# Kernel tuning notes

Hardware: AMD Instinct MI355X
Metric: run time of the kernel (lower is better)

Reference implementation:

```python
import jax, jax.numpy as jnp
import numpy as np

D_MODEL = 512
NHEAD = 8
MAX_REL = 256  # max_relative_position


def _linear(x, w, b):
    # torch nn.Linear: y = x @ W^T + b, W: [out, in]
    return jnp.einsum('...i,oi->...o', x, w) + b


def setup_inputs() -> dict:
    key = jax.random.key(0)
    ks = jax.random.split(key, 16)
    B, S, D = 32, 512, D_MODEL
    s = 0.02
    inp = {
        'query': jax.random.normal(ks[0], (B, S, D), jnp.float32),
        'key':   jax.random.normal(ks[1], (B, S, D), jnp.float32),
        'value': jax.random.normal(ks[2], (B, S, D), jnp.float32),
        # local attention projections (torch Linear weights [out,in])
        'wq': jax.random.normal(ks[3], (D, D), jnp.float32) * s,
        'bq': jnp.zeros((D,), jnp.float32),
        'wk': jax.random.normal(ks[4], (D, D), jnp.float32) * s,
        'bk': jnp.zeros((D,), jnp.float32),
        'wv': jax.random.normal(ks[5], (D, D), jnp.float32) * s,
        'bv': jnp.zeros((D,), jnp.float32),
        'wo': jax.random.normal(ks[6], (D, D), jnp.float32) * s,
        'bo': jnp.zeros((D,), jnp.float32),
        # relative-position key embedding table [2*MAX_REL+1, head_dim]
        'rel_k': jax.random.normal(ks[7], (2 * MAX_REL + 1, D // NHEAD), jnp.float32) * s,
        # global nn.MultiheadAttention (nhead//2 heads): packed in_proj + out_proj
        'g_in_w': jax.random.normal(ks[8], (3 * D, D), jnp.float32) * s,
        'g_in_b': jnp.zeros((3 * D,), jnp.float32),
        'g_out_w': jax.random.normal(ks[9], (D, D), jnp.float32) * s,
        'g_out_b': jnp.zeros((D,), jnp.float32),
    }
    return inp


def reference(query, key, value, wq, bq, wk, bk, wv, bv, wo, bo, rel_k,
              g_in_w, g_in_b, g_out_w, g_out_b):
    B, S, D = query.shape
    H, hd = NHEAD, D // NHEAD

    # --- local attention with relative-position bias ---
    q = _linear(query, wq, bq).reshape(B, S, H, hd).transpose(0, 2, 1, 3)  # [B,H,S,hd]
    k = _linear(key,   wk, bk).reshape(B, S, H, hd).transpose(0, 2, 1, 3)
    v = _linear(value, wv, bv).reshape(B, S, H, hd).transpose(0, 2, 1, 3)

    scores = jnp.einsum('bhqd,bhkd->bhqk', q, k) / jnp.sqrt(jnp.float32(hd))

    # relative positions: distance[i,j] = j - i, clamped, shifted to [0, 2*MAX_REL]
    idx = jnp.arange(S)
    rel_ids = jnp.clip(idx[None, :] - idx[:, None], -MAX_REL, MAX_REL) + MAX_REL  # [S,S]
    rel_pos_k = rel_k[rel_ids]  # [S, S, hd]
    scores = scores + jnp.einsum('bhld,lrd->bhlr', q, rel_pos_k)

    attn = jax.nn.softmax(scores, axis=-1)
    local = jnp.einsum('bhqk,bhkd->bhqd', attn, v)
    local = local.transpose(0, 2, 1, 3).reshape(B, S, D)

    # --- global MHA with H//2 heads ---
    Hg = H // 2
    hdg = D // Hg
    qg = _linear(query, g_in_w[:D], g_in_b[:D]).reshape(B, S, Hg, hdg).transpose(0, 2, 1, 3)
    kg = _linear(key,   g_in_w[D:2 * D], g_in_b[D:2 * D]).reshape(B, S, Hg, hdg).transpose(0, 2, 1, 3)
    vg = _linear(value, g_in_w[2 * D:], g_in_b[2 * D:]).reshape(B, S, Hg, hdg).transpose(0, 2, 1, 3)
    gs = jnp.einsum('bhqd,bhkd->bhqk', qg, kg) / jnp.sqrt(jnp.float32(hdg))
    ga = jax.nn.softmax(gs, axis=-1)
    g = jnp.einsum('bhqk,bhkd->bhqd', ga, vg).transpose(0, 2, 1, 3).reshape(B, S, D)
    g = _linear(g, g_out_w, g_out_b)

    combined = 0.7 * local + 0.3 * g
    return _linear(combined, wo, bo)
```

## Files before the change

### kernel.cpp

```cpp
#include <hip/hip_runtime.h>

typedef __attribute__((ext_vector_type(8))) short bh8;
typedef __attribute__((ext_vector_type(4))) float f4;

#define DEVI static __device__ __forceinline__

DEVI unsigned short f2b(float f) {
  union { float f; unsigned u; } v; v.f = f;
  unsigned r = v.u + 0x7fffu + ((v.u >> 16) & 1u);
  return (unsigned short)(r >> 16);
}
DEVI float b2f(unsigned short h) {
  union { unsigned u; float f; } v; v.u = ((unsigned)h) << 16;
  return v.f;
}
DEVI f4 mfma16(bh8 a, bh8 b, f4 c) {
  return __builtin_amdgcn_mfma_f32_16x16x32_bf16(a, b, c, 0, 0, 0);
}
DEVI void gload_lds16(const unsigned short* g, unsigned short* l) {
  __builtin_amdgcn_global_load_lds(
      (const __attribute__((address_space(1))) void*)(g),
      (__attribute__((address_space(3))) void*)(l), 16, 0, 0);
}

__global__ __launch_bounds__(256) void prep_all_kern(
    const float* __restrict__ q, const float* __restrict__ k, const float* __restrict__ v,
    const float* __restrict__ wq, const float* __restrict__ wk, const float* __restrict__ wv,
    const float* __restrict__ g_in_w, const float* __restrict__ g_out_w,
    const float* __restrict__ wo, const float* __restrict__ rel_k,
    const float* __restrict__ bgo, const float* __restrict__ bo,
    unsigned short* __restrict__ xq, unsigned short* __restrict__ xk, unsigned short* __restrict__ xv,
    unsigned short* __restrict__ Wq, unsigned short* __restrict__ Wk, unsigned short* __restrict__ Wv,
    unsigned short* __restrict__ Wo_, unsigned short* __restrict__ WgoT,
    unsigned short* __restrict__ Bfin, unsigned short* __restrict__ Rk,
    float* __restrict__ bias2) {
  if (blockIdx.x < 8192) {
    long i = ((long)blockIdx.x * 256 + threadIdx.x) * 4;
    float4 a = *(const float4*)(q + i);
    float4 b = *(const float4*)(k + i);
    float4 c = *(const float4*)(v + i);
    union { unsigned short s[4]; uint2 u; } pa, pb, pc;
    pa.s[0] = f2b(a.x); pa.s[1] = f2b(a.y); pa.s[2] = f2b(a.z); pa.s[3] = f2b(a.w);
    pb.s[0] = f2b(b.x); pb.s[1] = f2b(b.y); pb.s[2] = f2b(b.z); pb.s[3] = f2b(b.w);
    pc.s[0] = f2b(c.x); pc.s[1] = f2b(c.y); pc.s[2] = f2b(c.z); pc.s[3] = f2b(c.w);
    *(uint2*)(xq + i) = pa.u;
    *(uint2*)(xk + i) = pb.u;
    *(uint2*)(xv + i) = pc.u;
    return;
  }
  int bw = blockIdx.x - 8192;
  if (bw >= 2337) {
    int o = (bw - 2337) * 256 + threadIdx.x;
    if (o < 512) {
      const float* r = wo + (long)o * 512;
      float s = 0.f;
#pragma unroll 4
      for (int m = 0; m < 512; m += 4) {
        float4 a = *(const float4*)(r + m);
        float4 b = *(const float4*)(bgo + m);
        s += a.x * b.x + a.y * b.y + a.z * b.z + a.w * b.w;
      }
      bias2[o] = bo[o] + 0.3f * s;
    }
    return;
  }
  long i = ((long)bw * 256 + threadIdx.x) * 4;
  if (i >= 2392128L) return;
  if (i >= 2097152L && i < 2359296L) {
    long off = i - 2097152L;
    int ii = (int)(off >> 9), p = (int)(off & 511);
    union { unsigned short s[4]; uint2 u; } w;
#pragma unroll
    for (int tt = 0; tt < 4; tt++) w.s[tt] = f2b(g_out_w[(p + tt) * 512 + ii]);
    *(uint2*)(WgoT + off) = w.u;
    return;
  }
  const float* src; unsigned short* dst; long off; float sc = 1.0f;
  if (i < 524288L)        { dst = Wq;  off = i; src = (i < 262144L) ? wq + i : g_in_w + (i - 262144L); }
  else if (i < 1048576L)  { long j = i - 524288L;  dst = Wk;  off = j; src = (j < 262144L) ? wk + j : g_in_w + j; }
  else if (i < 1572864L)  { long j = i - 1048576L; dst = Wv;  off = j; src = (j < 262144L) ? wv + j : g_in_w + 262144L + j; }
  else if (i < 1835008L)  { long j = i - 1572864L; dst = Wo_; off = j; src = wo + j; }
  else if (i < 2097152L)  { long j = i - 1835008L; int col = (int)(j >> 9), kk = (int)(j & 511);
                            dst = Bfin; off = (long)col * 1024 + kk; src = wo + j; sc = 0.7f; }
  else                    { long j = i - 2359296L; dst = Rk;  off = j; src = rel_k + j; }
  float4 f = *(const float4*)src;
  union { unsigned short s[4]; uint2 u; } p;
  p.s[0] = f2b(f.x * sc); p.s[1] = f2b(f.y * sc); p.s[2] = f2b(f.z * sc); p.s[3] = f2b(f.w * sc);
  *(uint2*)(dst + off) = p.u;
}

__global__ __launch_bounds__(256) void gemm3_kern(
    const unsigned short* __restrict__ Xq, const unsigned short* __restrict__ Xk,
    const unsigned short* __restrict__ Xv,
    const unsigned short* __restrict__ Wq, const unsigned short* __restrict__ Wk,
    const unsigned short* __restrict__ Wv,
    const float* __restrict__ bq, const float* __restrict__ bk, const float* __restrict__ bv,
    const float* __restrict__ g_in_b,
    unsigned short* __restrict__ Yq, unsigned short* __restrict__ Yk_,
    unsigned short* __restrict__ Yvt_l, unsigned short* __restrict__ Yvt_g,
    const unsigned short* __restrict__ Wo_, const unsigned short* __restrict__ WgoT,
    unsigned short* __restrict__ Bfin) {
  __shared__ unsigned short lsA[128 * 64];
  __shared__ unsigned short lsB[128 * 64];
  const int t = threadIdx.x;
  const int lane = t & 63, w = t >> 6;
  const int l15 = lane & 15, g = lane >> 4, g4 = g * 4;
  const int n = blockIdx.x;

  const unsigned short *Ap, *Bp;
  const float *b0 = nullptr, *b1 = nullptr;
  int seg, rb, cb;
  if (n < 3072) {
    seg = n >> 10;
    int m = n & 1023;
    int x = m >> 3, c = m & 7;
    rb = (c * 16 + (x & 15)) * 128;
    cb = (x >> 4) * 128;
    Ap = (seg == 0) ? Xq : (seg == 1) ? Xk : Xv;
    Bp = (seg == 0) ? Wq : (seg == 1) ? Wk : Wv;
    b0 = (seg == 0) ? bq : (seg == 1) ? bk : bv;
    b1 = g_in_b + seg * 512;
  } else {
    seg = 3;
    int m2 = n - 3072;
    rb = (m2 & 3) * 128; cb = (m2 >> 2) * 128;
    Ap = Wo_; Bp = WgoT;
  }

  const int wr = (w >> 1) * 64, wc = (w & 1) * 64;
  const int tr = t >> 3;
  const int kci = ((t & 7) ^ (tr & 7)) * 8;
  const unsigned short* pa = Ap + (long)(rb + tr) * 512 + kci;
  const unsigned short* pb = Bp + (long)(cb + tr) * 512 + kci;

  f4 acc[4][4] = {};
  for (int k0 = 0; k0 < 512; k0 += 64) {
    __syncthreads();
#pragma unroll
    for (int p = 0; p < 4; p++) {
      gload_lds16(pa + k0 + (long)p * 32 * 512, lsA + p * 2048 + w * 512);
      gload_lds16(pb + k0 + (long)p * 32 * 512, lsB + p * 2048 + w * 512);
    }
    __syncthreads();
    bh8 af[2][4], bf[2][4];
#pragma unroll
    for (int kh = 0; kh < 2; kh++) {
#pragma unroll
      for (int m = 0; m < 4; m++) {
        int rl = wr + m * 16 + l15;
        af[kh][m] = *(const bh8*)(lsA + rl * 64 + (((kh * 4 + g) ^ (rl & 7)) * 8));
      }
#pragma unroll
      for (int nn = 0; nn < 4; nn++) {
        int rl = wc + nn * 16 + l15;
        bf[kh][nn] = *(const bh8*)(lsB + rl * 64 + (((kh * 4 + g) ^ (rl & 7)) * 8));
      }
    }
    __builtin_amdgcn_s_setprio(1);
#pragma unroll
    for (int m = 0; m < 4; m++)
#pragma unroll
      for (int nn = 0; nn < 4; nn++) {
        acc[m][nn] = mfma16(af[0][m], bf[0][nn], acc[m][nn]);
        acc[m][nn] = mfma16(af[1][m], bf[1][nn], acc[m][nn]);
      }
    __builtin_amdgcn_s_setprio(0);
  }

  if (seg == 3) {
#pragma unroll
    for (int m = 0; m < 4; m++)
#pragma unroll
      for (int nn = 0; nn < 4; nn++)
#pragma unroll
        for (int j = 0; j < 4; j++) {
          int row = rb + wr + m * 16 + g4 + j;
          int col = cb + wc + nn * 16 + l15;
          Bfin[(long)row * 1024 + 512 + col] = f2b(0.3f * acc[m][nn][j]);
        }
    return;
  }
  if (seg == 2) {
#pragma unroll
    for (int m = 0; m < 4; m++)
#pragma unroll
      for (int nn = 0; nn < 4; nn++) {
        int col = cb + wc + nn * 16 + l15;
        float bsv = (col < 512) ? b0[col] : b1[col - 512];
        unsigned r[4];
#pragma unroll
        for (int j = 0; j < 4; j++) {
          union { float f; unsigned u; } v; v.f = acc[m][nn][j] + bsv;
          r[j] = v.u + 0x7fffu + ((v.u >> 16) & 1u);
        }
        unsigned lo = (r[0] >> 16) | (r[1] & 0xffff0000u);
        unsigned hi = (r[2] >> 16) | (r[3] & 0xffff0000u);
        int row0 = rb + wr + m * 16 + g4;
        int bb = row0 >> 9, s = row0 & 511;
        if (col < 512) {
          int hh = col >> 6, d = col & 63;
          *(uint2*)(Yvt_l + (((long)(bb * 8 + hh) * 64 + d) << 9) + s) = make_uint2(lo, hi);
        } else {
          int c2 = col - 512, hg = c2 >> 7, dg = c2 & 127;
          *(uint2*)(Yvt_g + (((long)(bb * 4 + hg) * 128 + dg) << 9) + s) = make_uint2(lo, hi);
        }
      }
    return;
  }
  unsigned short* Yo = (seg == 0) ? Yq : Yk_;
#pragma unroll
  for (int m = 0; m < 4; m++)
#pragma unroll
    for (int nn = 0; nn < 4; nn++)
#pragma unroll
      for (int j = 0; j < 4; j++) {
        int row = rb + wr + m * 16 + g4 + j;
        int col = cb + wc + nn * 16 + l15;
        float v = acc[m][nn][j] + ((col < 512) ? b0[col] : b1[col - 512]);
        Yo[(long)row * 1024 + col] = f2b(v);
      }
}

__global__ __launch_bounds__(256) void gemm_fin_kern(
    const unsigned short* __restrict__ A, const unsigned short* __restrict__ Bw,
    const float* __restrict__ bias0, float* __restrict__ outf) {
  __shared__ unsigned short lsA[128 * 64];
  __shared__ unsigned short lsB[128 * 64];
  const int t = threadIdx.x;
  const int lane = t & 63, w = t >> 6;
  const int l15 = lane & 15, g = lane >> 4, g4 = g * 4;
  int n = blockIdx.x;
  int x = n >> 3, c = n & 7;
  const int rb = (c * 16 + (x & 15)) * 128;
  const int cb = (x >> 4) * 128;
  const int wr = (w >> 1) * 64, wc = (w & 1) * 64;
  const int tr = t >> 3;
  const int kci = ((t & 7) ^ (tr & 7)) * 8;

  const unsigned short* pa = A + (long)(rb + tr) * 1024 + kci;
  const unsigned short* pb = Bw + (long)(cb + tr) * 1024 + kci;

  f4 acc[4][4] = {};
  for (int k0 = 0; k0 < 1024; k0 += 64) {
    __syncthreads();
#pragma unroll
    for (int p = 0; p < 4; p++) {
      gload_lds16(pa + k0 + (long)p * 32 * 1024, lsA + p * 2048 + w * 512);
      gload_lds16(pb + k0 + (long)p * 32 * 1024, lsB + p * 2048 + w * 512);
    }
    __syncthreads();
    bh8 af[2][4], bf[2][4];
#pragma unroll
    for (int kh = 0; kh < 2; kh++) {
#pragma unroll
      for (int m = 0; m < 4; m++) {
        int rl = wr + m * 16 + l15;
        af[kh][m] = *(const bh8*)(lsA + rl * 64 + (((kh * 4 + g) ^ (rl & 7)) * 8));
      }
#pragma unroll
      for (int nn = 0; nn < 4; nn++) {
        int rl = wc + nn * 16 + l15;
        bf[kh][nn] = *(const bh8*)(lsB + rl * 64 + (((kh * 4 + g) ^ (rl & 7)) * 8));
      }
    }
    __builtin_amdgcn_s_setprio(1);
#pragma unroll
    for (int m = 0; m < 4; m++)
#pragma unroll
      for (int nn = 0; nn < 4; nn++) {
        acc[m][nn] = mfma16(af[0][m], bf[0][nn], acc[m][nn]);
        acc[m][nn] = mfma16(af[1][m], bf[1][nn], acc[m][nn]);
      }
    __builtin_amdgcn_s_setprio(0);
  }
#pragma unroll
  for (int m = 0; m < 4; m++)
#pragma unroll
    for (int nn = 0; nn < 4; nn++)
#pragma unroll
      for (int j = 0; j < 4; j++) {
        int row = rb + wr + m * 16 + g4 + j;
        int col = cb + wc + nn * 16 + l15;
        outf[(long)row * 512 + col] = acc[m][nn][j] + bias0[col];
      }
}

__global__ __launch_bounds__(512, 4) void attn_local_kern(
    const unsigned short* __restrict__ Yq, const unsigned short* __restrict__ Yk,
    const unsigned short* __restrict__ Yvt, const unsigned short* __restrict__ relk,
    unsigned short* __restrict__ outC) {
  __shared__ unsigned short kv[2][8192];
  __shared__ unsigned short buf[32 * 524];
  __shared__ float redbuf[8][32];

  const int t = threadIdx.x, lane = t & 63, w = t >> 6;
  const int l15 = lane & 15, g = lane >> 4, g8 = g * 8;
  int n = blockIdx.x;
  int bid = (n & 7) * 512 + (n >> 3);
  const int qt = bid & 15;
  const int h = (bid >> 4) & 7;
  const int b = bid >> 7;
  const int qb = qt * 32;
  const long base = ((long)(b * 512)) * 1024 + h * 64;
  const long vbase = ((long)(b * 8 + h)) * 64 * 512;

#define STAGE_K(ROFF, BUF) { \
    const int c_ = t & 7; \
    _Pragma("unroll") \
    for (int it = 0; it < 2; it++) { \
      int rr = it * 64 + (t >> 3); \
      gload_lds16(Yk + base + (long)((ROFF) + rr) * 1024 + ((c_ ^ (rr & 7)) * 8), \
                  kv[BUF] + it * 4096 + w * 512); \
    } }
#define STAGE_V(COFF, BUF) { \
    const int c_ = t & 15; \
    _Pragma("unroll") \
    for (int it = 0; it < 2; it++) { \
      int dd_ = it * 32 + (t >> 4); \
      gload_lds16(Yvt + vbase + (long)dd_ * 512 + (COFF) + ((c_ ^ (dd_ & 15)) * 8), \
                  kv[BUF] + it * 4096 + w * 512); \
    } }
#define QK(CH) { \
    int rl = w * 16 + l15; \
    const unsigned short* kb_ = kv[(CH) & 1]; \
    bh8 k0 = *(const bh8*)(kb_ + rl * 64 + ((g ^ (rl & 7)) * 8)); \
    bh8 k1 = *(const bh8*)(kb_ + rl * 64 + (((g + 4) ^ (rl & 7)) * 8)); \
    _Pragma("unroll") \
    for (int mm = 0; mm < 2; mm++) { \
      f4 a = {}; \
      a = mfma16(qf[mm][0], k0, a); \
      a = mfma16(qf[mm][1], k1, a); \
      sc[mm][CH] = a; \
    } }
#define GATHER(CH) { \
    _Pragma("unroll") \
    for (int mm = 0; mm < 2; mm++) \
    _Pragma("unroll") \
    for (int j = 0; j < 4; j++) { \
      int lr = mm * 16 + g * 4 + j; \
      int rowb = lr * 524; \
      int idx = rowb + 256 - (qb + lr) + (CH) * 128 + w * 16 + l15; \
      idx = idx < rowb ? rowb : idx; \
      idx = idx > rowb + 512 ? rowb + 512 : idx; \
      float p = exp2f(fmaf(sc[mm][CH][j], 0.18033688011112042f, b2f(buf[idx]))); \
      sc[mm][CH][j] = p; \
      rs[mm][j] += p; \
    } }

  STAGE_K(0, 0);

  bh8 qf[2][2];
#pragma unroll
  for (int mm = 0; mm < 2; mm++) {
    const unsigned short* qp = Yq + base + (long)(qb + mm * 16 + l15) * 1024 + g8;
    qf[mm][0] = *(const bh8*)(qp);
    qf[mm][1] = *(const bh8*)(qp + 32);
  }

  for (int tt = w; tt < 33; tt += 8) {
    int ri = tt * 16 + l15; if (ri > 512) ri = 512;
    const unsigned short* rp = relk + ri * 64 + g8;
    bh8 rf0 = *(const bh8*)(rp), rf1 = *(const bh8*)(rp + 32);
    int col = tt * 16 + l15;
#pragma unroll
    for (int mm = 0; mm < 2; mm++) {
      f4 a = {};
      a = mfma16(qf[mm][0], rf0, a);
      a = mfma16(qf[mm][1], rf1, a);
      if (col < 524) {
#pragma unroll
        for (int j = 0; j < 4; j++)
          buf[(mm * 16 + g * 4 + j) * 524 + col] = f2b(a[j] * 1.4426950408889634f);
      }
    }
  }
  __syncthreads();

  f4 sc[2][4];
  float rs[2][4] = {};

#pragma unroll
  for (int c = 0; c < 4; c++) {
    if (c < 3) { STAGE_K((c + 1) * 128, (c + 1) & 1); }
    else       { STAGE_V(0, 0); }
    __builtin_amdgcn_s_setprio(1);
    QK(c);
    __builtin_amdgcn_s_setprio(0);
    GATHER(c);
    __syncthreads();
  }

#pragma unroll
  for (int mm = 0; mm < 2; mm++)
#pragma unroll
    for (int j = 0; j < 4; j++) {
      int lr = mm * 16 + g * 4 + j;
      float s = rs[mm][j];
      for (int d = 1; d < 16; d <<= 1) s += __shfl_xor(s, d, 64);
      if (l15 == 0) redbuf[w][lr] = s;
    }
#pragma unroll
  for (int mm = 0; mm < 2; mm++)
#pragma unroll
    for (int ch = 0; ch < 4; ch++) {
      int col = ch * 128 + w * 16 + l15;
#pragma unroll
      for (int j = 0; j < 4; j++)
        buf[(mm * 16 + g * 4 + j) * 524 + col] = f2b(sc[mm][ch][j]);
    }
  __syncthreads();

  const int mmw = w >> 2, dt = w & 3;
  const int dd = dt * 16 + l15;
  float rinvj[4];
#pragma unroll
  for (int j = 0; j < 4; j++) {
    int lr = mmw * 16 + g * 4 + j;
    float s = 0.f;
#pragma unroll
    for (int ww = 0; ww < 8; ww++) s += redbuf[ww][lr];
    rinvj[j] = __builtin_amdgcn_rcpf(s);
  }

  f4 accO = {};
#pragma unroll
  for (int d = 0; d < 4; d++) {
    if (d < 3) { STAGE_V((d + 1) * 128, (d + 1) & 1); }
    const unsigned short* vb_ = kv[d & 1];
    __builtin_amdgcn_s_setprio(1);
#pragma unroll
    for (int ks2 = 0; ks2 < 4; ks2++) {
      union { uint2 u[2]; bh8 v; } pa;
      const unsigned short* pp = buf + (mmw * 16 + l15) * 524 + (d * 4 + ks2) * 32 + g8;
      pa.u[0] = *(const uint2*)(pp);
      pa.u[1] = *(const uint2*)(pp + 4);
      bh8 vv = *(const bh8*)(vb_ + dd * 128 + (((ks2 * 4 + g) ^ (dd & 15)) * 8));
      accO = mfma16(pa.v, vv, accO);
    }
    __builtin_amdgcn_s_setprio(0);
    if (d < 3) __syncthreads();
  }
#pragma unroll
  for (int j = 0; j < 4; j++) {
    int row = qb + mmw * 16 + g * 4 + j;
    outC[((long)(b * 512 + row)) * 1024 + h * 64 + dt * 16 + l15] = f2b(accO[j] * rinvj[j]);
  }
#undef STAGE_K
#undef STAGE_V
#undef QK
#undef GATHER
}

__global__ __launch_bounds__(512, 4) void attn_glob_kern(
    const unsigned short* __restrict__ Yq, const unsigned short* __restrict__ Yk,
    const unsigned short* __restrict__ Yvt, unsigned short* __restrict__ outC) {
  __shared__ unsigned short kv[2][8192];
  __shared__ unsigned short buf[32 * 520];
  __shared__ float redbuf[8][32];

  const int t = threadIdx.x, lane = t & 63, w = t >> 6;
  const int l15 = lane & 15, g = lane >> 4, g8 = g * 8;
  int n = blockIdx.x;
  int bid = (n & 7) * 256 + (n >> 3);
  const int qt = bid & 15;
  const int hg = (bid >> 4) & 3;
  const int b = bid >> 6;
  const int qb = qt * 32;
  const long base = ((long)(b * 512)) * 1024 + 512 + hg * 128;
  const long vgbase = ((long)(b * 4 + hg)) * 128 * 512;

#define STAGE_GK(KC, BUF) { \
    const int c_ = t & 15; \
    _Pragma("unroll") \
    for (int it = 0; it < 2; it++) { \
      int rr = it * 32 + (t >> 4); \
      gload_lds16(Yk + base + (long)((KC) * 64 + rr) * 1024 + ((c_ ^ (rr & 15)) * 8), \
                  kv[BUF] + it * 4096 + w * 512); \
    } }
#define STAGE_GV(KC, BUF) { \
    const int c_ = t & 7; \
    _Pragma("unroll") \
    for (int it = 0; it < 2; it++) { \
      int dd_ = it * 64 + (t >> 3); \
      gload_lds16(Yvt + vgbase + (long)dd_ * 512 + (KC) * 64 + ((c_ ^ (dd_ & 7)) * 8), \
                  kv[BUF] + it * 4096 + w * 512); \
    } }

  const int mmq = w >> 2, wq4 = w & 3;

  STAGE_GK(0, 0);

  bh8 qf[4];
  {
    const unsigned short* qp = Yq + base + (long)(qb + mmq * 16 + l15) * 1024 + g8;
#pragma unroll
    for (int ks = 0; ks < 4; ks++) qf[ks] = *(const bh8*)(qp + ks * 32);
  }
  __syncthreads();

  f4 sc8[8];
#pragma unroll
  for (int kc = 0; kc < 8; kc++) {
    if (kc < 7) { STAGE_GK(kc + 1, (kc + 1) & 1); }
    else        { STAGE_GV(0, 0); }
    const unsigned short* kb_ = kv[kc & 1];
    const int rl = wq4 * 16 + l15;
    __builtin_amdgcn_s_setprio(1);
    f4 a = {};
#pragma unroll
    for (int ks = 0; ks < 4; ks++) {
      bh8 kf = *(const bh8*)(kb_ + rl * 128 + (((ks * 4 + g) ^ (rl & 15)) * 8));
      a = mfma16(qf[ks], kf, a);
    }
    sc8[kc] = a;
    __builtin_amdgcn_s_setprio(0);
    __syncthreads();
  }

#pragma unroll
  for (int j = 0; j < 4; j++) {
    int lr = mmq * 16 + g * 4 + j;
    float s = 0.f;
#pragma unroll
    for (int kc = 0; kc < 8; kc++) {
      float p = exp2f(sc8[kc][j] * 0.12751745334f);
      sc8[kc][j] = p;
      s += p;
    }
    for (int d = 1; d < 16; d <<= 1) s += __shfl_xor(s, d, 64);
    if (l15 == 0) redbuf[w][lr] = s;
  }
  __syncthreads();

#pragma unroll
  for (int kc = 0; kc < 8; kc++) {
    int col = kc * 64 + wq4 * 16 + l15;
#pragma unroll
    for (int j = 0; j < 4; j++)
      buf[(mmq * 16 + g * 4 + j) * 520 + col] = f2b(sc8[kc][j]);
  }
  float rinv[2][4];
#pragma unroll
  for (int mm = 0; mm < 2; mm++)
#pragma unroll
    for (int j = 0; j < 4; j++) {
      int lr = mm * 16 + g * 4 + j;
      float s = redbuf[mm * 4 + 0][lr] + redbuf[mm * 4 + 1][lr] +
                redbuf[mm * 4 + 2][lr] + redbuf[mm * 4 + 3][lr];
      rinv[mm][j] = __builtin_amdgcn_rcpf(s);
    }
  __syncthreads();

  const int dd = w * 16 + l15;
  f4 accO[2] = {};
#pragma unroll
  for (int kc = 0; kc < 8; kc++) {
    if (kc < 7) { STAGE_GV(kc + 1, (kc + 1) & 1); }
    const unsigned short* vb_ = kv[kc & 1];
    __builtin_amdgcn_s_setprio(1);
#pragma unroll
    for (int ks2 = 0; ks2 < 2; ks2++) {
      bh8 vv = *(const bh8*)(vb_ + dd * 64 + (((ks2 * 4 + g) ^ (dd & 7)) * 8));
#pragma unroll
      for (int mm = 0; mm < 2; mm++) {
        union { uint2 u[2]; bh8 v; } pa;
        const unsigned short* pp = buf + (mm * 16 + l15) * 520 + kc * 64 + ks2 * 32 + g8;
        pa.u[0] = *(const uint2*)(pp);
        pa.u[1] = *(const uint2*)(pp + 4);
        accO[mm] = mfma16(pa.v, vv, accO[mm]);
      }
    }
    __builtin_amdgcn_s_setprio(0);
    if (kc < 7) __syncthreads();
  }
#pragma unroll
  for (int mm = 0; mm < 2; mm++)
#pragma unroll
    for (int j = 0; j < 4; j++) {
      int row = qb + mm * 16 + g * 4 + j;
      outC[((long)(b * 512 + row)) * 1024 + 512 + hg * 128 + w * 16 + l15] = f2b(accO[mm][j] * rinv[mm][j]);
    }
#undef STAGE_GK
#undef STAGE_GV
}

extern "C" void kernel_launch(void* const* d_in, const int* in_sizes, int n_in,
                              void* d_out, int out_size, void* d_ws, size_t ws_size,
                              hipStream_t stream) {
  const float* query = (const float*)d_in[0];
  const float* key   = (const float*)d_in[1];
  const float* value = (const float*)d_in[2];
  const float* wq = (const float*)d_in[3];   const float* bq = (const float*)d_in[4];
  const float* wk = (const float*)d_in[5];   const float* bk = (const float*)d_in[6];
  const float* wv = (const float*)d_in[7];   const float* bv = (const float*)d_in[8];
  const float* wo = (const float*)d_in[9];   const float* bo = (const float*)d_in[10];
  const float* rel_k = (const float*)d_in[11];
  const float* g_in_w = (const float*)d_in[12];  const float* g_in_b = (const float*)d_in[13];
  const float* g_out_w = (const float*)d_in[14]; const float* g_out_b = (const float*)d_in[15];

  unsigned short* p = (unsigned short*)d_ws;
  unsigned short* Xq = p;            p += 8388608;
  unsigned short* Xk = p;            p += 8388608;
  unsigned short* Xv = p;            p += 8388608;
  unsigned short* Yq = p;            p += 16777216;
  unsigned short* Yk = p;            p += 16777216;
  unsigned short* Yvt_l = p;         p += 8388608;
  unsigned short* Yvt_g = p;         p += 8388608;
  unsigned short* Wq = p;            p += 524288;
  unsigned short* Wk = p;            p += 524288;
  unsigned short* Wv = p;            p += 524288;
  unsigned short* Wo_ = p;           p += 262144;
  unsigned short* WgoT = p;          p += 262144;
  unsigned short* Bfin = p;          p += 524288;
  unsigned short* Rk = p;            p += 32832;
  float* bias2 = (float*)p;          p += 1024;
  unsigned short* CAT = Xq;

  prep_all_kern<<<10531, 256, 0, stream>>>(query, key, value,
                                           wq, wk, wv, g_in_w, g_out_w, wo, rel_k,
                                           g_out_b, bo,
                                           Xq, Xk, Xv, Wq, Wk, Wv, Wo_, WgoT, Bfin, Rk, bias2);

  gemm3_kern<<<3088, 256, 0, stream>>>(Xq, Xk, Xv, Wq, Wk, Wv, bq, bk, bv, g_in_b,
                                       Yq, Yk, Yvt_l, Yvt_g, Wo_, WgoT, Bfin);

  attn_local_kern<<<4096, 512, 0, stream>>>(Yq, Yk, Yvt_l, Rk, CAT);
  attn_glob_kern<<<2048, 512, 0, stream>>>(Yq, Yk, Yvt_g, CAT);

  gemm_fin_kern<<<512, 256, 0, stream>>>(CAT, Bfin, bias2, (float*)d_out);
}
```

Measured before the change: 299.4 us.

## Halve K/V LDS staging chunks and remap warps to raise local-attention occupancy

The local attention kernel now stages K and V in 64-row chunks instead of 128, which halves the double-buffered LDS footprint. Warps are remapped so each handles one 16-row query tile across 4 column groups, cutting per-thread score registers. Launch bounds go from 4 to 6 blocks per CU to use the freed LDS and registers. The cost is twice as many pipeline stages and __syncthreads barriers, with less work between them.

```diff
diff --git a/kernel.cpp b/kernel.cpp
--- a/kernel.cpp
+++ b/kernel.cpp
@@ -285,11 +285,11 @@
       }
 }
 
-__global__ __launch_bounds__(512, 4) void attn_local_kern(
+__global__ __launch_bounds__(512, 6) void attn_local_kern(
     const unsigned short* __restrict__ Yq, const unsigned short* __restrict__ Yk,
     const unsigned short* __restrict__ Yvt, const unsigned short* __restrict__ relk,
     unsigned short* __restrict__ outC) {
-  __shared__ unsigned short kv[2][8192];
+  __shared__ unsigned short kv[2][4096];
   __shared__ unsigned short buf[32 * 524];
   __shared__ float redbuf[8][32];
 
@@ -303,85 +303,69 @@
   const int qb = qt * 32;
   const long base = ((long)(b * 512)) * 1024 + h * 64;
   const long vbase = ((long)(b * 8 + h)) * 64 * 512;
+  const int mmq = w >> 2, wq4 = w & 3;
 
 #define STAGE_K(ROFF, BUF) { \
-    const int c_ = t & 7; \
-    _Pragma("unroll") \
-    for (int it = 0; it < 2; it++) { \
-      int rr = it * 64 + (t >> 3); \
-      gload_lds16(Yk + base + (long)((ROFF) + rr) * 1024 + ((c_ ^ (rr & 7)) * 8), \
-                  kv[BUF] + it * 4096 + w * 512); \
-    } }
-#define STAGE_V(COFF, BUF) { \
-    const int c_ = t & 15; \
-    _Pragma("unroll") \
-    for (int it = 0; it < 2; it++) { \
-      int dd_ = it * 32 + (t >> 4); \
-      gload_lds16(Yvt + vbase + (long)dd_ * 512 + (COFF) + ((c_ ^ (dd_ & 15)) * 8), \
-                  kv[BUF] + it * 4096 + w * 512); \
-    } }
+    int rr = t >> 3, c_ = t & 7; \
+    gload_lds16(Yk + base + (long)((ROFF) + rr) * 1024 + ((c_ ^ (rr & 7)) * 8), \
+                kv[BUF] + w * 512); }
+#define STAGE_V(KC, BUF) { \
+    int dd_ = t >> 3, c_ = t & 7; \
+    gload_lds16(Yvt + vbase + (long)dd_ * 512 + (KC) * 64 + ((c_ ^ (dd_ & 7)) * 8), \
+                kv[BUF] + w * 512); }
 #define QK(CH) { \
-    int rl = w * 16 + l15; \
+    int rl = wq4 * 16 + l15; \
     const unsigned short* kb_ = kv[(CH) & 1]; \
     bh8 k0 = *(const bh8*)(kb_ + rl * 64 + ((g ^ (rl & 7)) * 8)); \
     bh8 k1 = *(const bh8*)(kb_ + rl * 64 + (((g + 4) ^ (rl & 7)) * 8)); \
-    _Pragma("unroll") \
-    for (int mm = 0; mm < 2; mm++) { \
-      f4 a = {}; \
-      a = mfma16(qf[mm][0], k0, a); \
-      a = mfma16(qf[mm][1], k1, a); \
-      sc[mm][CH] = a; \
-    } }
+    f4 a = {}; \
+    a = mfma16(qfm[0], k0, a); \
+    a = mfma16(qfm[1], k1, a); \
+    sc8[CH] = a; }
 #define GATHER(CH) { \
     _Pragma("unroll") \
-    for (int mm = 0; mm < 2; mm++) \
-    _Pragma("unroll") \
     for (int j = 0; j < 4; j++) { \
-      int lr = mm * 16 + g * 4 + j; \
+      int lr = mmq * 16 + g * 4 + j; \
       int rowb = lr * 524; \
-      int idx = rowb + 256 - (qb + lr) + (CH) * 128 + w * 16 + l15; \
+      int idx = rowb + 256 - (qb + lr) + (CH) * 64 + wq4 * 16 + l15; \
       idx = idx < rowb ? rowb : idx; \
       idx = idx > rowb + 512 ? rowb + 512 : idx; \
-      float p = exp2f(fmaf(sc[mm][CH][j], 0.18033688011112042f, b2f(buf[idx]))); \
-      sc[mm][CH][j] = p; \
-      rs[mm][j] += p; \
+      float p = exp2f(fmaf(sc8[CH][j], 0.18033688011112042f, b2f(buf[idx]))); \
+      sc8[CH][j] = p; \
+      rs[j] += p; \
     } }
 
   STAGE_K(0, 0);
 
-  bh8 qf[2][2];
-#pragma unroll
-  for (int mm = 0; mm < 2; mm++) {
-    const unsigned short* qp = Yq + base + (long)(qb + mm * 16 + l15) * 1024 + g8;
-    qf[mm][0] = *(const bh8*)(qp);
-    qf[mm][1] = *(const bh8*)(qp + 32);
-  }
-
-  for (int tt = w; tt < 33; tt += 8) {
+  bh8 qfm[2];
+  {
+    const unsigned short* qp = Yq + base + (long)(qb + mmq * 16 + l15) * 1024 + g8;
+    qfm[0] = *(const bh8*)(qp);
+    qfm[1] = *(const bh8*)(qp + 32);
+  }
+
+  for (int tt = wq4; tt < 33; tt += 4) {
     int ri = tt * 16 + l15; if (ri > 512) ri = 512;
     const unsigned short* rp = relk + ri * 64 + g8;
     bh8 rf0 = *(const bh8*)(rp), rf1 = *(const bh8*)(rp + 32);
+    f4 a = {};
+    a = mfma16(qfm[0], rf0, a);
+    a = mfma16(qfm[1], rf1, a);
     int col = tt * 16 + l15;
-#pragma unroll
-    for (int mm = 0; mm < 2; mm++) {
-      f4 a = {};
-      a = mfma16(qf[mm][0], rf0, a);
-      a = mfma16(qf[mm][1], rf1, a);
-      if (col < 524) {
-#pragma unroll
-        for (int j = 0; j < 4; j++)
-          buf[(mm * 16 + g * 4 + j) * 524 + col] = f2b(a[j] * 1.4426950408889634f);
-      }
+    if (col < 524) {
+#pragma unroll
+      for (int j = 0; j < 4; j++)
+        buf[(mmq * 16 + g * 4 + j) * 524 + col] = f2b(a[j] * 1.4426950408889634f);
     }
   }
   __syncthreads();
 
-  f4 sc[2][4];
-  float rs[2][4] = {};
-
-#pragma unroll
-  for (int c = 0; c < 4; c++) {
-    if (c < 3) { STAGE_K((c + 1) * 128, (c + 1) & 1); }
+  f4 sc8[8];
+  float rs[4] = {};
+
+#pragma unroll
+  for (int c = 0; c < 8; c++) {
+    if (c < 7) { STAGE_K((c + 1) * 64, (c + 1) & 1); }
     else       { STAGE_V(0, 0); }
     __builtin_amdgcn_s_setprio(1);
     QK(c);
@@ -391,23 +375,19 @@
   }
 
 #pragma unroll
-  for (int mm = 0; mm < 2; mm++)
-#pragma unroll
-    for (int j = 0; j < 4; j++) {
-      int lr = mm * 16 + g * 4 + j;
-      float s = rs[mm][j];
-      for (int d = 1; d < 16; d <<= 1) s += __shfl_xor(s, d, 64);
-      if (l15 == 0) redbuf[w][lr] = s;
-    }
-#pragma unroll
-  for (int mm = 0; mm < 2; mm++)
-#pragma unroll
-    for (int ch = 0; ch < 4; ch++) {
-      int col = ch * 128 + w * 16 + l15;
-#pragma unroll
-      for (int j = 0; j < 4; j++)
-        buf[(mm * 16 + g * 4 + j) * 524 + col] = f2b(sc[mm][ch][j]);
-    }
+  for (int j = 0; j < 4; j++) {
+    int lr = mmq * 16 + g * 4 + j;
+    float s = rs[j];
+    for (int d = 1; d < 16; d <<= 1) s += __shfl_xor(s, d, 64);
+    if (l15 == 0) redbuf[w][lr] = s;
+  }
+#pragma unroll
+  for (int ch = 0; ch < 8; ch++) {
+    int col = ch * 64 + wq4 * 16 + l15;
+#pragma unroll
+    for (int j = 0; j < 4; j++)
+      buf[(mmq * 16 + g * 4 + j) * 524 + col] = f2b(sc8[ch][j]);
+  }
   __syncthreads();
 
   const int mmw = w >> 2, dt = w & 3;
@@ -416,29 +396,28 @@
 #pragma unroll
   for (int j = 0; j < 4; j++) {
     int lr = mmw * 16 + g * 4 + j;
-    float s = 0.f;
-#pragma unroll
-    for (int ww = 0; ww < 8; ww++) s += redbuf[ww][lr];
+    float s = redbuf[mmw * 4 + 0][lr] + redbuf[mmw * 4 + 1][lr] +
+              redbuf[mmw * 4 + 2][lr] + redbuf[mmw * 4 + 3][lr];
     rinvj[j] = __builtin_amdgcn_rcpf(s);
   }
 
   f4 accO = {};
 #pragma unroll
-  for (int d = 0; d < 4; d++) {
-    if (d < 3) { STAGE_V((d + 1) * 128, (d + 1) & 1); }
-    const unsigned short* vb_ = kv[d & 1];
+  for (int kc = 0; kc < 8; kc++) {
+    if (kc < 7) { STAGE_V(kc + 1, (kc + 1) & 1); }
+    const unsigned short* vb_ = kv[kc & 1];
     __builtin_amdgcn_s_setprio(1);
 #pragma unroll
-    for (int ks2 = 0; ks2 < 4; ks2++) {
+    for (int ks2 = 0; ks2 < 2; ks2++) {
       union { uint2 u[2]; bh8 v; } pa;
-      const unsigned short* pp = buf + (mmw * 16 + l15) * 524 + (d * 4 + ks2) * 32 + g8;
+      const unsigned short* pp = buf + (mmw * 16 + l15) * 524 + kc * 64 + ks2 * 32 + g8;
       pa.u[0] = *(const uint2*)(pp);
       pa.u[1] = *(const uint2*)(pp + 4);
-      bh8 vv = *(const bh8*)(vb_ + dd * 128 + (((ks2 * 4 + g) ^ (dd & 15)) * 8));
+      bh8 vv = *(const bh8*)(vb_ + dd * 64 + (((ks2 * 4 + g) ^ (dd & 7)) * 8));
       accO = mfma16(pa.v, vv, accO);
     }
     __builtin_amdgcn_s_setprio(0);
-    if (d < 3) __syncthreads();
+    if (kc < 7) __syncthreads();
   }
 #pragma unroll
   for (int j = 0; j < 4; j++) {
```

Result: no change. 305.4 us (+2.0%).
